# Performance work log

Measured on AMD Instinct MI355X. Metric: run time of the kernel, lower is better.

## Reference

```python
import math
import jax, jax.numpy as jnp
import numpy as np

K = 8
D = 8
LAMBDA_PRIOR = 0.01
TRI = D * (D + 1) // 2  # 36
PHI_DIM = K + K * D + K * TRI  # 360
_ROWS, _COLS = np.tril_indices(D)


def _unpack_phi(phi):
    # phi: [M, PHI_DIM] -> pi_tilde [M,K], mu [M,K,D], L_vecs [M,K,TRI]
    M = phi.shape[0]
    pi_tilde = phi[:, :K]
    mu = phi[:, K:K + K * D].reshape(M, K, D)
    L_vecs = phi[:, K + K * D:].reshape(M, K, TRI)
    return pi_tilde, mu, L_vecs


def _L_vec_to_matrix(L_vecs):
    # L_vecs: [M,K,TRI] -> lower-triangular L [M,K,D,D]
    M, Kc, _ = L_vecs.shape
    L = jnp.zeros((M, Kc, D, D), dtype=L_vecs.dtype)
    return L.at[:, :, _ROWS, _COLS].set(L_vecs)


def _gmm_log_likelihood(phi, X):
    # phi: [M, PHI_DIM], X: [N, D] -> log_lik [M]
    pi_tilde, mu, L_vecs = _unpack_phi(phi)
    log_pi = jax.nn.log_softmax(pi_tilde, axis=-1)          # [M,K]
    L = _L_vec_to_matrix(L_vecs)                             # [M,K,D,D]
    diff = X[None, None, :, :] - mu[:, :, None, :]           # [M,K,N,D]
    diff_T = jnp.swapaxes(diff, -1, -2)                      # [M,K,D,N]
    # solve L alpha = diff_T for each (m,k); batched triangular solve
    alpha = jax.scipy.linalg.solve_triangular(L, diff_T, lower=True)  # [M,K,D,N]
    maha = jnp.sum(alpha * alpha, axis=-2)                   # [M,K,N]
    log_diag = jnp.log(jnp.clip(jnp.abs(jnp.diagonal(L, axis1=-2, axis2=-1)), 1e-8))
    log_det = 2.0 * jnp.sum(log_diag, axis=-1)               # [M,K]
    log_norm_const = -0.5 * (D * math.log(2 * math.pi) + log_det[:, :, None])
    log_gauss = log_norm_const - 0.5 * maha                  # [M,K,N]
    log_mix = jax.scipy.special.logsumexp(log_pi[:, :, None] + log_gauss, axis=1)  # [M,N]
    return jnp.sum(log_mix, axis=-1)                         # [M]


def setup_inputs() -> dict:
    key = jax.random.key(0)
    k1, k2 = jax.random.split(key)
    M, N = 32, 32768
    phi = jax.random.normal(k1, (M, PHI_DIM), dtype=jnp.float32)
    X = jax.random.normal(k2, (N, D), dtype=jnp.float32)
    return {"phi": phi, "X": X}


def reference(phi, X):
    # U(phi; X) = -log p(X|phi) + lambda_prior * ||phi||^2 / 2  -> [M]
    log_lik = _gmm_log_likelihood(phi, X)
    prior = 0.5 * jnp.sum(phi * phi, axis=-1)
    return -log_lik + LAMBDA_PRIOR * prior
```

## Files before the change

kernel.cpp:

```cpp
#include <hip/hip_runtime.h>
#include <math.h>

#define KK 8
#define DD 8
#define TRI 36
#define PHI_DIM 360
#define MM 32
#define NN 32768
#define GX 32
#define TPB 256
#define PP 4

__launch_bounds__(TPB)
__global__ void gmm_kernel(const float* __restrict__ phi, const float* __restrict__ X,
                           float* __restrict__ out) {
    __shared__ float s_par[KK][48];
    __shared__ float s_red[TPB / 64];

    const int m = blockIdx.y;
    const float* __restrict__ ph = phi + m * PHI_DIM;
    const int tid = threadIdx.x;

    if (tid < KK) {
        const int k = tid;
        #pragma unroll
        for (int i = 0; i < DD; i++) s_par[k][i] = ph[KK + k * DD + i];
        #pragma unroll
        for (int t = 0; t < TRI; t++) s_par[k][8 + t] = ph[KK + KK * DD + k * TRI + t];
        float logdet = 0.f;
        #pragma unroll
        for (int i = 0; i < DD; i++) {
            const int di = 8 + i * (i + 1) / 2 + i;
            float dv = s_par[k][di];
            logdet += 2.f * __logf(fmaxf(fabsf(dv), 1e-8f));
            s_par[k][di] = 1.f / dv;
        }
        float mx = ph[0];
        #pragma unroll
        for (int i = 1; i < KK; i++) mx = fmaxf(mx, ph[i]);
        float sum = 0.f;
        #pragma unroll
        for (int i = 0; i < KK; i++) sum += __expf(ph[i] - mx);
        const float lse = mx + __logf(sum);
        s_par[k][44] = (ph[k] - lse) - 0.5f * (8.f * 1.8378770664093453f + logdet);
    }

    float pr = 0.f;
    if (blockIdx.x == 0) {
        for (int j = tid; j < PHI_DIM; j += TPB) {
            float v = ph[j];
            pr = fmaf(v, v, pr);
        }
    }
    __syncthreads();

    const int n0 = blockIdx.x * (NN / GX) + tid;
    float x[PP][DD];
    #pragma unroll
    for (int p = 0; p < PP; p++) {
        const float4* xp = (const float4*)(X + (size_t)(n0 + p * TPB) * DD);
        float4 u0 = xp[0], u1 = xp[1];
        x[p][0] = u0.x; x[p][1] = u0.y; x[p][2] = u0.z; x[p][3] = u0.w;
        x[p][4] = u1.x; x[p][5] = u1.y; x[p][6] = u1.z; x[p][7] = u1.w;
    }

    float v[PP][KK];
    #pragma unroll
    for (int k = 0; k < KK; k++) {
        float par[45];
        #pragma unroll
        for (int t = 0; t < 45; t++) par[t] = s_par[k][t];

        #pragma unroll
        for (int p = 0; p < PP; p++) {
            float a[DD];
            float maha = 0.f;
            #pragma unroll
            for (int i = 0; i < DD; i++) {
                float t = x[p][i] - par[i];
                #pragma unroll
                for (int j = 0; j < i; j++)
                    t = fmaf(-par[8 + i * (i + 1) / 2 + j], a[j], t);
                a[i] = t * par[8 + i * (i + 1) / 2 + i];
                maha = fmaf(a[i], a[i], maha);
            }
            v[p][k] = par[44] - 0.5f * maha;
        }
    }

    float acc = 0.f;
    #pragma unroll
    for (int p = 0; p < PP; p++) {
        float mx = v[p][0];
        #pragma unroll
        for (int i = 1; i < KK; i++) mx = fmaxf(mx, v[p][i]);
        float s = 0.f;
        #pragma unroll
        for (int i = 0; i < KK; i++) s += __expf(v[p][i] - mx);
        acc += mx + __logf(s);
    }

    float contrib = 0.005f * pr - acc;

    #pragma unroll
    for (int off = 32; off; off >>= 1) contrib += __shfl_down(contrib, off, 64);
    if ((tid & 63) == 0) s_red[tid >> 6] = contrib;
    __syncthreads();
    if (tid == 0) {
        float t = s_red[0] + s_red[1] + s_red[2] + s_red[3];
        atomicAdd(&out[m], t);
    }
}

extern "C" void kernel_launch(void* const* d_in, const int* in_sizes, int n_in,
                              void* d_out, int out_size, void* d_ws, size_t ws_size,
                              hipStream_t stream) {
    const float* phi = (const float*)d_in[0];
    const float* X   = (const float*)d_in[1];
    float* out = (float*)d_out;

    hipMemsetAsync(out, 0, out_size * sizeof(float), stream);
    dim3 grid(GX, MM);
    gmm_kernel<<<grid, TPB, 0, stream>>>(phi, X, out);
}
```

Before: 72.10 us.

## Precompute precision-matrix quadratic form in setup kernel, fold log2e into coefficients

Adds a small setup kernel that inverts each Cholesky factor, forms the precision matrix, and writes per-component quadratic, linear and constant coefficients, pre-scaled by log2(e), to workspace. The main kernel then evaluates each Gaussian log-density as a direct quadratic form in x and uses exp2/log2. This removes the per-sample triangular solve with its serial dependency chain, and the setup kernel also replaces the memset and initialises the output with the prior term. In exchange it adds an extra kernel launch, and expanding the quadratic form may lose some precision through cancellation.

```diff
diff --git a/kernel.cpp b/kernel.cpp
--- a/kernel.cpp
+++ b/kernel.cpp
@@ -10,47 +10,123 @@
 #define GX 32
 #define TPB 256
 #define PP 4
+#define CSTRIDE 48
+
+#define LOG2E 1.4426950408889634f
+#define LN2   0.6931471805599453f
+
+__global__ void setup_kernel(const float* __restrict__ phi, float* __restrict__ ws,
+                             float* __restrict__ out) {
+    const int m = blockIdx.x;
+    const float* __restrict__ ph = phi + m * PHI_DIM;
+    const int lane = threadIdx.x;
+
+    float pr = 0.f;
+    for (int j = lane; j < PHI_DIM; j += 64) { float v = ph[j]; pr = fmaf(v, v, pr); }
+    #pragma unroll
+    for (int off = 32; off; off >>= 1) pr += __shfl_down(pr, off, 64);
+    if (lane == 0) out[m] = 0.005f * pr;
+
+    if (lane >= KK) return;
+    const int k = lane;
+
+    float pi0 = ph[0];
+    float mx = pi0;
+    #pragma unroll
+    for (int i = 1; i < KK; i++) mx = fmaxf(mx, ph[i]);
+    float se = 0.f;
+    #pragma unroll
+    for (int i = 0; i < KK; i++) se += __expf(ph[i] - mx);
+    const float lp = ph[k] - (mx + __logf(se));
+
+    float mu[DD];
+    #pragma unroll
+    for (int i = 0; i < DD; i++) mu[i] = ph[KK + k * DD + i];
+
+    float Lm[DD][DD];
+    #pragma unroll
+    for (int i = 0; i < DD; i++)
+        #pragma unroll
+        for (int j = 0; j <= i; j++)
+            Lm[i][j] = ph[KK + KK * DD + k * TRI + i * (i + 1) / 2 + j];
+
+    float logdet = 0.f;
+    #pragma unroll
+    for (int i = 0; i < DD; i++)
+        logdet += 2.f * __logf(fmaxf(fabsf(Lm[i][i]), 1e-8f));
+
+    float Li[DD][DD];
+    #pragma unroll
+    for (int i = 0; i < DD; i++) {
+        const float r = 1.f / Lm[i][i];
+        Li[i][i] = r;
+        #pragma unroll
+        for (int j = 0; j < i; j++) {
+            float s = 0.f;
+            #pragma unroll
+            for (int p = 0; p < DD; p++)
+                if (p >= j && p < i) s = fmaf(Lm[i][p], Li[p][j], s);
+            Li[i][j] = -r * s;
+        }
+    }
+
+    float P[DD][DD];
+    #pragma unroll
+    for (int i = 0; i < DD; i++)
+        #pragma unroll
+        for (int j = 0; j <= i; j++) {
+            float s = 0.f;
+            #pragma unroll
+            for (int p = 0; p < DD; p++)
+                if (p >= i) s = fmaf(Li[p][i], Li[p][j], s);
+            P[i][j] = s;
+        }
+
+    float b[DD];
+    #pragma unroll
+    for (int i = 0; i < DD; i++) {
+        float s = 0.f;
+        #pragma unroll
+        for (int j = 0; j < DD; j++) {
+            float pij = (j <= i) ? P[i][j] : P[j][i];
+            s = fmaf(pij, mu[j], s);
+        }
+        b[i] = s;
+    }
+    float c0 = 0.f;
+    #pragma unroll
+    for (int i = 0; i < DD; i++) c0 = fmaf(b[i], mu[i], c0);
+
+    const float C = lp - 0.5f * (8.f * 1.8378770664093453f + logdet) - 0.5f * c0;
+
+    float* __restrict__ row = ws + (size_t)(m * KK + k) * CSTRIDE;
+    #pragma unroll
+    for (int i = 0; i < DD; i++) row[i] = b[i] * LOG2E;
+    #pragma unroll
+    for (int i = 0; i < DD; i++)
+        #pragma unroll
+        for (int j = 0; j <= i; j++) {
+            float g = (j == i) ? -0.5f * P[i][i] : -P[i][j];
+            row[8 + i * (i + 1) / 2 + j] = g * LOG2E;
+        }
+    row[44] = C * LOG2E;
+    row[45] = 0.f; row[46] = 0.f; row[47] = 0.f;
+}
 
 __launch_bounds__(TPB)
-__global__ void gmm_kernel(const float* __restrict__ phi, const float* __restrict__ X,
+__global__ void gmm_kernel(const float* __restrict__ ws, const float* __restrict__ X,
                            float* __restrict__ out) {
-    __shared__ float s_par[KK][48];
+    __shared__ float s_c[KK][CSTRIDE];
     __shared__ float s_red[TPB / 64];
 
     const int m = blockIdx.y;
-    const float* __restrict__ ph = phi + m * PHI_DIM;
     const int tid = threadIdx.x;
 
-    if (tid < KK) {
-        const int k = tid;
-        #pragma unroll
-        for (int i = 0; i < DD; i++) s_par[k][i] = ph[KK + k * DD + i];
-        #pragma unroll
-        for (int t = 0; t < TRI; t++) s_par[k][8 + t] = ph[KK + KK * DD + k * TRI + t];
-        float logdet = 0.f;
-        #pragma unroll
-        for (int i = 0; i < DD; i++) {
-            const int di = 8 + i * (i + 1) / 2 + i;
-            float dv = s_par[k][di];
-            logdet += 2.f * __logf(fmaxf(fabsf(dv), 1e-8f));
-            s_par[k][di] = 1.f / dv;
-        }
-        float mx = ph[0];
-        #pragma unroll
-        for (int i = 1; i < KK; i++) mx = fmaxf(mx, ph[i]);
-        float sum = 0.f;
-        #pragma unroll
-        for (int i = 0; i < KK; i++) sum += __expf(ph[i] - mx);
-        const float lse = mx + __logf(sum);
-        s_par[k][44] = (ph[k] - lse) - 0.5f * (8.f * 1.8378770664093453f + logdet);
-    }
-
-    float pr = 0.f;
-    if (blockIdx.x == 0) {
-        for (int j = tid; j < PHI_DIM; j += TPB) {
-            float v = ph[j];
-            pr = fmaf(v, v, pr);
-        }
+    {
+        const float* __restrict__ src = ws + (size_t)m * KK * CSTRIDE;
+        #pragma unroll
+        for (int j = tid; j < KK * CSTRIDE; j += TPB)
+            ((float*)s_c)[j] = src[j];
     }
     __syncthreads();
 
@@ -67,28 +143,26 @@
     float v[PP][KK];
     #pragma unroll
     for (int k = 0; k < KK; k++) {
-        float par[45];
-        #pragma unroll
-        for (int t = 0; t < 45; t++) par[t] = s_par[k][t];
+        float cf[45];
+        #pragma unroll
+        for (int t = 0; t < 45; t++) cf[t] = s_c[k][t];
 
         #pragma unroll
         for (int p = 0; p < PP; p++) {
-            float a[DD];
-            float maha = 0.f;
+            float vv = cf[44];
             #pragma unroll
             for (int i = 0; i < DD; i++) {
-                float t = x[p][i] - par[i];
+                float inner = cf[i];
                 #pragma unroll
-                for (int j = 0; j < i; j++)
-                    t = fmaf(-par[8 + i * (i + 1) / 2 + j], a[j], t);
-                a[i] = t * par[8 + i * (i + 1) / 2 + i];
-                maha = fmaf(a[i], a[i], maha);
+                for (int j = 0; j <= i; j++)
+                    inner = fmaf(cf[8 + i * (i + 1) / 2 + j], x[p][j], inner);
+                vv = fmaf(x[p][i], inner, vv);
             }
-            v[p][k] = par[44] - 0.5f * maha;
-        }
-    }
-
-    float acc = 0.f;
+            v[p][k] = vv;
+        }
+    }
+
+    float acc2 = 0.f;
     #pragma unroll
     for (int p = 0; p < PP; p++) {
         float mx = v[p][0];
@@ -96,11 +170,11 @@
         for (int i = 1; i < KK; i++) mx = fmaxf(mx, v[p][i]);
         float s = 0.f;
         #pragma unroll
-        for (int i = 0; i < KK; i++) s += __expf(v[p][i] - mx);
-        acc += mx + __logf(s);
-    }
-
-    float contrib = 0.005f * pr - acc;
+        for (int i = 0; i < KK; i++) s += __builtin_exp2f(v[p][i] - mx);
+        acc2 += mx + __builtin_log2f(s);
+    }
+
+    float contrib = -acc2 * LN2;
 
     #pragma unroll
     for (int off = 32; off; off >>= 1) contrib += __shfl_down(contrib, off, 64);
@@ -118,8 +192,9 @@
     const float* phi = (const float*)d_in[0];
     const float* X   = (const float*)d_in[1];
     float* out = (float*)d_out;
-
-    hipMemsetAsync(out, 0, out_size * sizeof(float), stream);
+    float* ws  = (float*)d_ws;
+
+    setup_kernel<<<MM, 64, 0, stream>>>(phi, ws, out);
     dim3 grid(GX, MM);
-    gmm_kernel<<<grid, TPB, 0, stream>>>(phi, X, out);
+    gmm_kernel<<<grid, TPB, 0, stream>>>(ws, X, out);
 }
```

Result: slower. 75.38 us (+4.6%).
